# Performance work log

Hardware: AMD Instinct MI355X
Metric: run time of the kernel (lower is better)

## Reference

```python
import jax, jax.numpy as jnp
import numpy as np

GRID_EXTENT = 80.0  # world coords in [0, 80) per the t[0]*(W/80.0) mapping


def setup_inputs() -> dict:
    key = jax.random.key(0)
    k1, k2 = jax.random.split(key)
    B, C, H, W, N = 16, 8, 512, 512, 64
    preds = jax.random.normal(k1, (B, C, H, W), dtype=jnp.float32)
    # targets: (B, N, 7); coords t[...,0], t[...,1] in [0, 80)
    targets = jax.random.uniform(k2, (B, N, 7), dtype=jnp.float32) * GRID_EXTENT
    return {"preds": preds, "targets": targets}


def _build_maps(targets, B, H, W):
    # grid indices: int(clamp(t * (W/80), 0, W-1)) -- truncation == floor for nonneg
    gx = jnp.clip(targets[..., 0] * (W / GRID_EXTENT), 0, W - 1).astype(jnp.int32)  # (B,N)
    gy = jnp.clip(targets[..., 1] * (H / GRID_EXTENT), 0, H - 1).astype(jnp.int32)  # (B,N)
    b = jnp.broadcast_to(jnp.arange(B)[:, None], gx.shape)                           # (B,N)
    # vectorized scatter replacing the per-target Python loop
    tm = jnp.zeros((B, H, W, 7), targets.dtype).at[b, gy, gx].set(targets)  # (B,H,W,7)
    mask = jnp.zeros((B, H, W), targets.dtype).at[b, gy, gx].set(1.0)       # (B,H,W)
    return jnp.transpose(tm, (0, 3, 1, 2)), mask  # (B,7,H,W), (B,H,W)


def reference(preds, targets):
    B, _, H, W = preds.shape
    cls_preds = preds[:, 0]    # (B,H,W) logits
    reg_preds = preds[:, 1:]   # (B,7,H,W)
    target_map, mask = _build_maps(targets, B, H, W)

    # BCEWithLogitsLoss(reduction='mean'), numerically stable form
    x, z = cls_preds, mask
    cls_loss = jnp.mean(jnp.maximum(x, 0.0) - x * z + jnp.log1p(jnp.exp(-jnp.abs(x))))

    num_objects = mask.sum()

    # SmoothL1 (beta=1), reduction='none', masked mean over positive cells
    d = reg_preds - target_map
    ad = jnp.abs(d)
    sl1 = jnp.where(ad < 1.0, 0.5 * d * d, ad - 0.5)
    reg_loss = (sl1 * mask[:, None, :, :]).sum() / (num_objects + 1e-6)
    reg_loss = jnp.where(num_objects > 0, reg_loss, 0.0)

    total_loss = cls_loss + 2.0 * reg_loss
    return total_loss, num_objects
```

## Files before the change

kernel.cpp:

```cpp
#include <hip/hip_runtime.h>

#define B_   16
#define HW_  (512 * 512)
#define BHW  (B_ * HW_)
#define NT   1024
#define SCALE (512.0f / 80.0f)

#define NB1  1024
#define BLK  256

__device__ __forceinline__ float block_reduce_sum(float v, float* smem) {
    #pragma unroll
    for (int off = 32; off > 0; off >>= 1) v += __shfl_down(v, off);
    int lane = threadIdx.x & 63, wid = threadIdx.x >> 6;
    if (lane == 0) smem[wid] = v;
    __syncthreads();
    if (wid == 0) {
        v = (lane < (BLK >> 6)) ? smem[lane] : 0.0f;
        #pragma unroll
        for (int off = 32; off > 0; off >>= 1) v += __shfl_down(v, off);
    }
    return v;
}

__global__ __launch_bounds__(BLK) void sp_partial(
        const float* __restrict__ preds,
        float* __restrict__ part) {
    __shared__ float smem[BLK / 64];
    const float4* p4 = (const float4*)preds;
    const int tid = blockIdx.x * BLK + threadIdx.x;
    float local = 0.0f;
    #pragma unroll
    for (int k = 0; k < 4; ++k) {
        int i   = tid + k * (NB1 * BLK);
        int b   = i >> 16;
        int rem = i & 0xFFFF;
        float4 v = p4[((size_t)b << 19) + rem];
        local += fmaxf(v.x, 0.0f) + __logf(1.0f + __expf(-fabsf(v.x)));
        local += fmaxf(v.y, 0.0f) + __logf(1.0f + __expf(-fabsf(v.y)));
        local += fmaxf(v.z, 0.0f) + __logf(1.0f + __expf(-fabsf(v.z)));
        local += fmaxf(v.w, 0.0f) + __logf(1.0f + __expf(-fabsf(v.w)));
    }
    float s = block_reduce_sum(local, smem);
    if (threadIdx.x == 0) part[blockIdx.x] = s;
}

__global__ __launch_bounds__(BLK) void finalize_kernel(
        const float* __restrict__ preds,
        const float* __restrict__ targets,
        const float* __restrict__ part,
        float* __restrict__ out) {
    __shared__ float smem[BLK / 64];
    __shared__ int   cell[NT];

    float ps = 0.0f;
    #pragma unroll
    for (int k = 0; k < NB1 / BLK; ++k) ps += part[threadIdx.x + k * BLK];

    for (int t = threadIdx.x; t < NT; t += BLK) {
        float tx = targets[t * 7 + 0];
        float ty = targets[t * 7 + 1];
        int gx = (int)fminf(fmaxf(tx * SCALE, 0.0f), 511.0f);
        int gy = (int)fminf(fmaxf(ty * SCALE, 0.0f), 511.0f);
        cell[t] = gy * 512 + gx;
    }
    __syncthreads();

    float sum_x = 0.0f, reg = 0.0f, nobj = 0.0f;
    for (int t = threadIdx.x; t < NT; t += BLK) {
        int b = t >> 6, n = t & 63;
        int c = cell[t];
        bool win = true;
        for (int n2 = n + 1; n2 < 64; ++n2) {
            if (cell[(b << 6) + n2] == c) { win = false; break; }
        }
        if (win) {
            nobj += 1.0f;
            size_t base = ((size_t)b << 21) + (size_t)c;
            sum_x += preds[base];
            #pragma unroll
            for (int ch = 0; ch < 7; ++ch) {
                float d  = preds[base + ((size_t)(ch + 1) << 18)]
                         - targets[t * 7 + ch];
                float ad = fabsf(d);
                reg += (ad < 1.0f) ? 0.5f * d * d : ad - 0.5f;
            }
        }
    }

    float rps = block_reduce_sum(ps, smem);
    __syncthreads();
    float rs = block_reduce_sum(sum_x, smem);
    __syncthreads();
    float rr = block_reduce_sum(reg, smem);
    __syncthreads();
    float rn = block_reduce_sum(nobj, smem);

    if (threadIdx.x == 0) {
        float cls = (rps - rs) / (float)BHW;
        float rl  = (rn > 0.0f) ? rr / (rn + 1e-6f) : 0.0f;
        out[0] = cls + 2.0f * rl;
        out[1] = rn;
    }
}

extern "C" void kernel_launch(void* const* d_in, const int* in_sizes, int n_in,
                              void* d_out, int out_size, void* d_ws, size_t ws_size,
                              hipStream_t stream) {
    const float* preds   = (const float*)d_in[0];
    const float* targets = (const float*)d_in[1];
    float* out  = (float*)d_out;
    float* part = (float*)d_ws;

    sp_partial<<<NB1, BLK, 0, stream>>>(preds, part);
    finalize_kernel<<<1, BLK, 0, stream>>>(preds, targets, part, out);
}
```

Baseline: 199.5 us.

## Move per-target gather into main grid as extra blocks, slim finalize kernel

The scattered per-target regression gathers and the dedup scan move out of the single-block finalize kernel into 16 extra blocks of the main kernel, one per batch. In each of those blocks the 8 channel loads are split across 4 wave groups. This takes the latency-bound gather off the serial tail so it overlaps with the streaming softplus reduction. The finalize kernel then only sums partials, at the cost of a larger workspace layout and a branch in the main kernel.

```diff
diff --git a/kernel.cpp b/kernel.cpp
--- a/kernel.cpp
+++ b/kernel.cpp
@@ -3,11 +3,11 @@
 #define B_   16
 #define HW_  (512 * 512)
 #define BHW  (B_ * HW_)
-#define NT   1024
 #define SCALE (512.0f / 80.0f)
 
 #define NB1  1024
 #define BLK  256
+
 
 __device__ __forceinline__ float block_reduce_sum(float v, float* smem) {
     #pragma unroll
@@ -23,78 +23,105 @@
     return v;
 }
 
-__global__ __launch_bounds__(BLK) void sp_partial(
-        const float* __restrict__ preds,
-        float* __restrict__ part) {
-    __shared__ float smem[BLK / 64];
-    const float4* p4 = (const float4*)preds;
-    const int tid = blockIdx.x * BLK + threadIdx.x;
-    float local = 0.0f;
-    #pragma unroll
-    for (int k = 0; k < 4; ++k) {
-        int i   = tid + k * (NB1 * BLK);
-        int b   = i >> 16;
-        int rem = i & 0xFFFF;
-        float4 v = p4[((size_t)b << 19) + rem];
-        local += fmaxf(v.x, 0.0f) + __logf(1.0f + __expf(-fabsf(v.x)));
-        local += fmaxf(v.y, 0.0f) + __logf(1.0f + __expf(-fabsf(v.y)));
-        local += fmaxf(v.z, 0.0f) + __logf(1.0f + __expf(-fabsf(v.z)));
-        local += fmaxf(v.w, 0.0f) + __logf(1.0f + __expf(-fabsf(v.w)));
-    }
-    float s = block_reduce_sum(local, smem);
-    if (threadIdx.x == 0) part[blockIdx.x] = s;
-}
-
-__global__ __launch_bounds__(BLK) void finalize_kernel(
+__global__ __launch_bounds__(BLK) void det_main(
         const float* __restrict__ preds,
         const float* __restrict__ targets,
-        const float* __restrict__ part,
-        float* __restrict__ out) {
+        float* __restrict__ ws) {
     __shared__ float smem[BLK / 64];
-    __shared__ int   cell[NT];
 
-    float ps = 0.0f;
-    #pragma unroll
-    for (int k = 0; k < NB1 / BLK; ++k) ps += part[threadIdx.x + k * BLK];
+    if (blockIdx.x < NB1) {
+        const float4* p4 = (const float4*)preds;
+        const int tid = blockIdx.x * BLK + threadIdx.x;
+        float local = 0.0f;
+        #pragma unroll
+        for (int k = 0; k < 4; ++k) {
+            int i   = tid + k * (NB1 * BLK);
+            int b   = i >> 16;
+            int rem = i & 0xFFFF;
+            float4 v = p4[((size_t)b << 19) + rem];
+            local += fmaxf(v.x, 0.0f) + __logf(1.0f + __expf(-fabsf(v.x)));
+            local += fmaxf(v.y, 0.0f) + __logf(1.0f + __expf(-fabsf(v.y)));
+            local += fmaxf(v.z, 0.0f) + __logf(1.0f + __expf(-fabsf(v.z)));
+            local += fmaxf(v.w, 0.0f) + __logf(1.0f + __expf(-fabsf(v.w)));
+        }
+        float s = block_reduce_sum(local, smem);
+        if (threadIdx.x == 0) ws[blockIdx.x] = s;
+        return;
+    }
 
-    for (int t = threadIdx.x; t < NT; t += BLK) {
+    __shared__ int cell[64];
+    const int b = blockIdx.x - NB1;
+    const int n = threadIdx.x & 63;
+    const int g = threadIdx.x >> 6;
+    const int t = (b << 6) + n;
+
+    if (g == 0) {
         float tx = targets[t * 7 + 0];
         float ty = targets[t * 7 + 1];
         int gx = (int)fminf(fmaxf(tx * SCALE, 0.0f), 511.0f);
         int gy = (int)fminf(fmaxf(ty * SCALE, 0.0f), 511.0f);
-        cell[t] = gy * 512 + gx;
+        cell[n] = gy * 512 + gx;
     }
     __syncthreads();
 
+    int c = cell[n];
+    bool win = true;
+    for (int n2 = n + 1; n2 < 64; ++n2) {
+        if (cell[n2] == c) { win = false; break; }
+    }
+
     float sum_x = 0.0f, reg = 0.0f, nobj = 0.0f;
-    for (int t = threadIdx.x; t < NT; t += BLK) {
-        int b = t >> 6, n = t & 63;
-        int c = cell[t];
-        bool win = true;
-        for (int n2 = n + 1; n2 < 64; ++n2) {
-            if (cell[(b << 6) + n2] == c) { win = false; break; }
-        }
-        if (win) {
-            nobj += 1.0f;
-            size_t base = ((size_t)b << 21) + (size_t)c;
-            sum_x += preds[base];
-            #pragma unroll
-            for (int ch = 0; ch < 7; ++ch) {
-                float d  = preds[base + ((size_t)(ch + 1) << 18)]
-                         - targets[t * 7 + ch];
+    if (win) {
+        size_t base = ((size_t)b << 21) + (size_t)c;
+        if (g == 0) nobj = 1.0f;
+        #pragma unroll
+        for (int j = 0; j < 2; ++j) {
+            int L = 2 * g + j;
+            float p = preds[base + ((size_t)L << 18)];
+            if (L == 0) {
+                sum_x = p;
+            } else {
+                float d  = p - targets[t * 7 + (L - 1)];
                 float ad = fabsf(d);
                 reg += (ad < 1.0f) ? 0.5f * d * d : ad - 0.5f;
             }
         }
     }
 
-    float rps = block_reduce_sum(ps, smem);
-    __syncthreads();
     float rs = block_reduce_sum(sum_x, smem);
     __syncthreads();
     float rr = block_reduce_sum(reg, smem);
     __syncthreads();
     float rn = block_reduce_sum(nobj, smem);
+    if (threadIdx.x == 0) {
+        ws[NB1 + b * 3 + 0] = rs;
+        ws[NB1 + b * 3 + 1] = rr;
+        ws[NB1 + b * 3 + 2] = rn;
+    }
+}
+
+__global__ __launch_bounds__(BLK) void det_finalize(
+        const float* __restrict__ ws,
+        float* __restrict__ out) {
+    __shared__ float smem[BLK / 64];
+    const float4* w4 = (const float4*)ws;
+    float4 v = w4[threadIdx.x];
+    float ps = v.x + v.y + v.z + v.w;
+
+    float sx = 0.0f, rg = 0.0f, nb = 0.0f;
+    if (threadIdx.x < 16) {
+        sx = ws[NB1 + threadIdx.x * 3 + 0];
+        rg = ws[NB1 + threadIdx.x * 3 + 1];
+        nb = ws[NB1 + threadIdx.x * 3 + 2];
+    }
+
+    float rps = block_reduce_sum(ps, smem);
+    __syncthreads();
+    float rs = block_reduce_sum(sx, smem);
+    __syncthreads();
+    float rr = block_reduce_sum(rg, smem);
+    __syncthreads();
+    float rn = block_reduce_sum(nb, smem);
 
     if (threadIdx.x == 0) {
         float cls = (rps - rs) / (float)BHW;
@@ -109,9 +136,9 @@
                               hipStream_t stream) {
     const float* preds   = (const float*)d_in[0];
     const float* targets = (const float*)d_in[1];
-    float* out  = (float*)d_out;
-    float* part = (float*)d_ws;
+    float* out = (float*)d_out;
+    float* ws  = (float*)d_ws;
 
-    sp_partial<<<NB1, BLK, 0, stream>>>(preds, part);
-    finalize_kernel<<<1, BLK, 0, stream>>>(preds, targets, part, out);
+    det_main<<<NB1 + B_, BLK, 0, stream>>>(preds, targets, ws);
+    det_finalize<<<1, BLK, 0, stream>>>(ws, out);
 }
```

Result: faster. 171.0 us (-14.3%).
